# Performance work log

Hardware: AMD Instinct MI355X
Metric: run time of the kernel (lower is better)

## Reference

```python
import jax, jax.numpy as jnp
import numpy as np

B, S, H, DH = 1, 4096, 8, 40  # hardcoded in the original forward
D = H * DH  # 320

def setup_inputs() -> dict:
    key = jax.random.key(0)
    ks = jax.random.split(key, 6)
    s = 1.0 / np.sqrt(D)
    return {
        "x": jax.random.normal(ks[0], (B, S, D), dtype=jnp.float32),
        "Wq": jax.random.normal(ks[1], (D, D), dtype=jnp.float32) * s,
        "Wk": jax.random.normal(ks[2], (D, D), dtype=jnp.float32) * s,
        "Wv": jax.random.normal(ks[3], (D, D), dtype=jnp.float32) * s,
        "Wo": jax.random.normal(ks[4], (D, D), dtype=jnp.float32) * s,
        "bo": jnp.zeros((D,), dtype=jnp.float32),
    }

def reference(x, Wq, Wk, Wv, Wo, bo):
    scale = DH ** (-0.5)
    # nn.Linear(bias=False): y = x @ W^T. context = x (self-attention).
    q = x @ Wq.T
    k = x @ Wk.T
    v = x @ Wv.T
    # split heads: [B,S,D] -> [B*H, S, DH]
    def split_heads(t):
        return t.reshape(B, S, H, DH).transpose(0, 2, 1, 3).reshape(B * H, S, DH)
    q, k, v = split_heads(q), split_heads(k), split_heads(v)
    # fp32 QK^T (original forces float), softmax, AV
    sim = jnp.einsum('bid,bjd->bij', q.astype(jnp.float32), k.astype(jnp.float32)) * scale
    attn = jax.nn.softmax(sim, axis=-1)
    out = jnp.einsum('bij,bjd->bid', attn, v)
    # merge heads: [B*H, S, DH] -> [B, S, D]
    out = out.reshape(B, H, S, DH).transpose(0, 2, 1, 3).reshape(B, S, D)
    return out @ Wo.T + bo
```

## Files before the change

kernel.cpp:

```cpp
#include <hip/hip_runtime.h>
#include <math.h>


#define NS 4096
#define ND 320
#define SCALE2 0.2281101152f
#define HS48 196608
#define VTH 163840
#define XN 1310720
#define WN 102400

typedef __attribute__((ext_vector_type(8))) short bf16x8;
typedef __attribute__((ext_vector_type(16))) float f32x16;

static __device__ __forceinline__ unsigned short f2b(float f) {
  unsigned int u = __builtin_bit_cast(unsigned int, f);
  u += 0x7fffu + ((u >> 16) & 1u);
  return (unsigned short)(u >> 16);
}
static __device__ __forceinline__ unsigned int pk2rne(float a, float b) {
  return (unsigned int)f2b(a) | ((unsigned int)f2b(b) << 16);
}
static __device__ __forceinline__ unsigned int pk2t(float a, float b) {
  return __builtin_amdgcn_perm(__builtin_bit_cast(unsigned int, b),
                               __builtin_bit_cast(unsigned int, a), 0x07060302u);
}
static __device__ __forceinline__ bf16x8 ld8(const unsigned short* p) {
  union { uint2 u[2]; bf16x8 v; } c;
  c.u[0] = *(const uint2*)p;
  c.u[1] = *(const uint2*)(p + 4);
  return c.v;
}
static __device__ __forceinline__ void st16(unsigned short* p, uint4 v) {
  *(uint2*)p = make_uint2(v.x, v.y);
  *(uint2*)(p + 4) = make_uint2(v.z, v.w);
}

__global__ __launch_bounds__(256) void cvt_kernel(
    const float* __restrict__ x, const float* __restrict__ Wq,
    const float* __restrict__ Wk, const float* __restrict__ Wv,
    const float* __restrict__ Wo, unsigned short* __restrict__ dst) {
  int e = (blockIdx.x * 256 + threadIdx.x) * 4;
  const float* src; int off;
  if (e < XN)               { src = x;  off = e; }
  else if (e < XN + WN)     { src = Wq; off = e - XN; }
  else if (e < XN + 2 * WN) { src = Wk; off = e - XN - WN; }
  else if (e < XN + 3 * WN) { src = Wv; off = e - XN - 2 * WN; }
  else                      { src = Wo; off = e - XN - 3 * WN; }
  float4 v = *(const float4*)(src + off);
  *(uint2*)(dst + e) = make_uint2(pk2rne(v.x, v.y), pk2rne(v.z, v.w));
}

__global__ __launch_bounds__(256) void proj_qkv_kernel(
    const unsigned short* __restrict__ xb, const unsigned short* __restrict__ Wb,
    unsigned short* __restrict__ Qp, unsigned short* __restrict__ Kp,
    unsigned short* __restrict__ Vt) {
  const int z = blockIdx.z;
  const unsigned short* W = Wb + z * WN;
  __shared__ __align__(16) unsigned short As[64 * 36];
  __shared__ __align__(16) unsigned short Bs[64 * 36];
  const int t = threadIdx.x;
  const int w = t >> 6, l = t & 63, l31 = l & 31, hi = l >> 5;
  const int bm = blockIdx.x * 64, bn = blockIdx.y * 64;
  const int m0 = (w & 1) * 32, n0 = (w >> 1) * 32;
  f32x16 acc = {0,0,0,0,0,0,0,0,0,0,0,0,0,0,0,0};
  const int ar = t >> 2, ac = t & 3;
  const unsigned short* gA = xb + (bm + ar) * ND + ac * 8;
  const unsigned short* gB = W + (bn + ar) * ND + ac * 8;
  unsigned short* lA = As + ar * 36 + ac * 8;
  unsigned short* lB = Bs + ar * 36 + ac * 8;
  const unsigned short* af = As + (m0 + l31) * 36 + hi * 8;
  const unsigned short* bf = Bs + (n0 + l31) * 36 + hi * 8;
  for (int k0 = 0; k0 < ND; k0 += 32) {
    __syncthreads();
    uint4 a = *(const uint4*)gA;
    uint4 b = *(const uint4*)gB;
    st16(lA, a); st16(lB, b);
    gA += 32; gB += 32;
    __syncthreads();
    bf16x8 A0 = ld8(af), A1 = ld8(af + 16);
    bf16x8 B0 = ld8(bf), B1 = ld8(bf + 16);
    acc = __builtin_amdgcn_mfma_f32_32x32x16_bf16(A0, B0, acc, 0, 0, 0);
    acc = __builtin_amdgcn_mfma_f32_32x32x16_bf16(A1, B1, acc, 0, 0, 0);
  }
  const int j = bn + n0 + l31;
  const int h = j / 40, dh = j - h * 40;
  if (z < 2) {
    unsigned short* Y = (z == 0) ? Qp : Kp;
    const float sc = (z == 0) ? SCALE2 : 1.0f;
    const unsigned short padv = (z == 0) ? (unsigned short)0xC200u
                                         : (unsigned short)0x3F80u;
#pragma unroll
    for (int r = 0; r < 16; r++) {
      int row = bm + m0 + (r & 3) + 8 * (r >> 2) + 4 * hi;
      Y[h * HS48 + row * 48 + dh] = f2b(acc[r] * sc);
      if (dh < 8)
        Y[h * HS48 + row * 48 + 40 + dh] = (dh == 0) ? padv : (unsigned short)0;
    }
  } else {
#pragma unroll
    for (int r = 0; r < 16; r++) {
      int row = bm + m0 + (r & 3) + 8 * (r >> 2) + 4 * hi;
      Vt[h * VTH + dh * NS + row] = f2b(acc[r]);
    }
  }
}

__global__ __launch_bounds__(256, 4) void attn_kernel(
    const unsigned short* __restrict__ Qp, const unsigned short* __restrict__ Kp,
    const unsigned short* __restrict__ Vt, float* __restrict__ Op,
    float* __restrict__ Lp) {
  const int b = blockIdx.x;
  const int h = b & 7, ks = (b >> 3) & 3, qt = b >> 5;
  const int t = threadIdx.x;
  const int w = t >> 6, l = t & 63, l31 = l & 31, hi = l >> 5;
  __shared__ __align__(16) unsigned short Ks[128 * 68];
  __shared__ __align__(16) unsigned short Vs[48 * 132];
  if (t < 66) ((unsigned int*)(Vs + 40 * 132))[t] = 0x3F803F80u;

  const int kbase = ks * 1024;
  const int qbase = qt * 128 + w * 32;
  const unsigned short* qp = Qp + h * HS48 + (qbase + l31) * 48 + hi * 8;
  bf16x8 qf0 = *(const bf16x8*)qp;
  bf16x8 qf1 = *(const bf16x8*)(qp + 16);
  bf16x8 qf2 = *(const bf16x8*)(qp + 32);

  f32x16 oa0 = {0,0,0,0,0,0,0,0,0,0,0,0,0,0,0,0};
  f32x16 oa1 = {0,0,0,0,0,0,0,0,0,0,0,0,0,0,0,0};

  const int krow = t >> 1, khalf = t & 1;
  const unsigned short* gK = Kp + h * HS48 + (kbase + krow) * 48 + khalf * 24;
  unsigned short* lK = Ks + krow * 68 + khalf * 24;
  const int vg = t & 15;
  const int vr0 = t >> 4, vr1 = (t + 256) >> 4, vr2 = (t + 512) >> 4;
  const unsigned short* gV = Vt + h * VTH + kbase;

  for (int it = 0; it < 8; ++it) {
    __syncthreads();
    uint4 ka = *(const uint4*)gK;
    uint4 kb = *(const uint4*)(gK + 8);
    uint4 kc = *(const uint4*)(gK + 16);
    st16(lK, ka); st16(lK + 8, kb); st16(lK + 16, kc);
    uint4 v0 = *(const uint4*)(gV + vr0 * NS + vg * 8);
    uint4 v1 = *(const uint4*)(gV + vr1 * NS + vg * 8);
    st16(Vs + vr0 * 132 + vg * 8, v0);
    st16(Vs + vr1 * 132 + vg * 8, v1);
    if (t < 128) {
      uint4 v2 = *(const uint4*)(gV + vr2 * NS + vg * 8);
      st16(Vs + vr2 * 132 + vg * 8, v2);
    }
    gK += 128 * 48; gV += 128;
    __syncthreads();

#pragma unroll
    for (int half = 0; half < 2; ++half) {
      const unsigned short* kfb = Ks + (half * 64 + l31) * 68 + hi * 8;
      f32x16 s0 = {0,0,0,0,0,0,0,0,0,0,0,0,0,0,0,0};
      f32x16 s1 = {0,0,0,0,0,0,0,0,0,0,0,0,0,0,0,0};
      {
        bf16x8 k0 = ld8(kfb), k1 = ld8(kfb + 16), k2 = ld8(kfb + 32);
        s0 = __builtin_amdgcn_mfma_f32_32x32x16_bf16(k0, qf0, s0, 0, 0, 0);
        s0 = __builtin_amdgcn_mfma_f32_32x32x16_bf16(k1, qf1, s0, 0, 0, 0);
        s0 = __builtin_amdgcn_mfma_f32_32x32x16_bf16(k2, qf2, s0, 0, 0, 0);
      }
      {
        const unsigned short* kg = kfb + 32 * 68;
        bf16x8 k0 = ld8(kg), k1 = ld8(kg + 16), k2 = ld8(kg + 32);
        s1 = __builtin_amdgcn_mfma_f32_32x32x16_bf16(k0, qf0, s1, 0, 0, 0);
        s1 = __builtin_amdgcn_mfma_f32_32x32x16_bf16(k1, qf1, s1, 0, 0, 0);
        s1 = __builtin_amdgcn_mfma_f32_32x32x16_bf16(k2, qf2, s1, 0, 0, 0);
      }
      float p0[16], p1[16];
#pragma unroll
      for (int r = 0; r < 16; r++) {
        p0[r] = exp2f(s0[r]);
        p1[r] = exp2f(s1[r]);
      }
      unsigned int pw0[8], pw1[8];
#pragma unroll
      for (int g = 0; g < 4; g++) {
        pw0[2 * g]     = pk2t(p0[4 * g + 0], p0[4 * g + 1]);
        pw0[2 * g + 1] = pk2t(p0[4 * g + 2], p0[4 * g + 3]);
        pw1[2 * g]     = pk2t(p1[4 * g + 0], p1[4 * g + 1]);
        pw1[2 * g + 1] = pk2t(p1[4 * g + 2], p1[4 * g + 3]);
      }
      unsigned int s00 = hi ? pw0[0] : pw0[2], s01 = hi ? pw0[1] : pw0[3];
      unsigned int s02 = hi ? pw0[4] : pw0[6], s03 = hi ? pw0[5] : pw0[7];
      unsigned int s10 = hi ? pw1[0] : pw1[2], s11 = hi ? pw1[1] : pw1[3];
      unsigned int s12 = hi ? pw1[4] : pw1[6], s13 = hi ? pw1[5] : pw1[7];
      unsigned int r00 = __shfl_xor(s00, 32), r01 = __shfl_xor(s01, 32);
      unsigned int r02 = __shfl_xor(s02, 32), r03 = __shfl_xor(s03, 32);
      unsigned int r10 = __shfl_xor(s10, 32), r11 = __shfl_xor(s11, 32);
      unsigned int r12 = __shfl_xor(s12, 32), r13 = __shfl_xor(s13, 32);
      uint4 u0 = hi ? make_uint4(r00, r01, pw0[2], pw0[3])
                    : make_uint4(pw0[0], pw0[1], r00, r01);
      uint4 u1 = hi ? make_uint4(r02, r03, pw0[6], pw0[7])
                    : make_uint4(pw0[4], pw0[5], r02, r03);
      uint4 u2 = hi ? make_uint4(r10, r11, pw1[2], pw1[3])
                    : make_uint4(pw1[0], pw1[1], r10, r11);
      uint4 u3 = hi ? make_uint4(r12, r13, pw1[6], pw1[7])
                    : make_uint4(pw1[4], pw1[5], r12, r13);
      bf16x8 pf[4];
      pf[0] = __builtin_bit_cast(bf16x8, u0);
      pf[1] = __builtin_bit_cast(bf16x8, u1);
      pf[2] = __builtin_bit_cast(bf16x8, u2);
      pf[3] = __builtin_bit_cast(bf16x8, u3);

      const unsigned short* vfb = Vs + l31 * 132 + half * 64 + hi * 8;
      const unsigned short* vfb2 = Vs + (32 + (l31 & 15)) * 132 + half * 64 + hi * 8;
      const bf16x8 zf = {0, 0, 0, 0, 0, 0, 0, 0};
#pragma unroll
      for (int sub = 0; sub < 4; sub++) {
        bf16x8 vb0 = ld8(vfb + sub * 16);
        bf16x8 vb1t = ld8(vfb2 + sub * 16);
        bf16x8 vb1 = (l31 < 9) ? vb1t : zf;
        oa0 = __builtin_amdgcn_mfma_f32_32x32x16_bf16(pf[sub], vb0, oa0, 0, 0, 0);
        oa1 = __builtin_amdgcn_mfma_f32_32x32x16_bf16(pf[sub], vb1, oa1, 0, 0, 0);
      }
    }
  }
  float* opb = Op + ks * 1310720 + h * 163840;
  float* lpb = Lp + ks * 32768 + h * NS;
#pragma unroll
  for (int r = 0; r < 16; r++) {
    int qr = qbase + (r & 3) + 8 * (r >> 2) + 4 * hi;
    opb[qr * 40 + l31] = oa0[r];
    if (l31 < 8) opb[qr * 40 + 32 + l31] = oa1[r];
    if (l31 == 8) lpb[qr] = oa1[r];
  }
}

__global__ __launch_bounds__(256) void combine_kernel(
    const float* __restrict__ Op, const float* __restrict__ Lp,
    unsigned short* __restrict__ Xo) {
  int e = (blockIdx.x * 256 + threadIdx.x) * 2;
  int h = e / 163840;
  int r = e - h * 163840;
  int s = r / 40;
  int dh = r - s * 40;
  float2 a0 = *(const float2*)(Op + e);
  float2 a1 = *(const float2*)(Op + e + 1310720);
  float2 a2 = *(const float2*)(Op + e + 2621440);
  float2 a3 = *(const float2*)(Op + e + 3932160);
  int li = h * NS + s;
  float lsum = Lp[li] + Lp[li + 32768] + Lp[li + 65536] + Lp[li + 98304];
  float inv = 1.0f / lsum;
  float o0 = (a0.x + a1.x + a2.x + a3.x) * inv;
  float o1 = (a0.y + a1.y + a2.y + a3.y) * inv;
  *(unsigned int*)(Xo + s * ND + h * 40 + dh) = pk2rne(o0, o1);
}

__global__ __launch_bounds__(256) void proj_out_kernel(
    const unsigned short* __restrict__ Xo, const unsigned short* __restrict__ Wob,
    const float* __restrict__ bo, float* __restrict__ out) {
  __shared__ __align__(16) unsigned short As[64 * 36];
  __shared__ __align__(16) unsigned short Bs[64 * 36];
  const int t = threadIdx.x;
  const int w = t >> 6, l = t & 63, l31 = l & 31, hi = l >> 5;
  const int bm = blockIdx.x * 64, bn = blockIdx.y * 64;
  const int m0 = (w & 1) * 32, n0 = (w >> 1) * 32;
  f32x16 acc = {0,0,0,0,0,0,0,0,0,0,0,0,0,0,0,0};
  const int ar = t >> 2, ac = t & 3;
  const unsigned short* gA = Xo + (bm + ar) * ND + ac * 8;
  const unsigned short* gB = Wob + (bn + ar) * ND + ac * 8;
  unsigned short* lA = As + ar * 36 + ac * 8;
  unsigned short* lB = Bs + ar * 36 + ac * 8;
  const unsigned short* af = As + (m0 + l31) * 36 + hi * 8;
  const unsigned short* bf = Bs + (n0 + l31) * 36 + hi * 8;
  for (int k0 = 0; k0 < ND; k0 += 32) {
    __syncthreads();
    uint4 a = *(const uint4*)gA;
    uint4 b = *(const uint4*)gB;
    st16(lA, a); st16(lB, b);
    gA += 32; gB += 32;
    __syncthreads();
    bf16x8 A0 = ld8(af), A1 = ld8(af + 16);
    bf16x8 B0 = ld8(bf), B1 = ld8(bf + 16);
    acc = __builtin_amdgcn_mfma_f32_32x32x16_bf16(A0, B0, acc, 0, 0, 0);
    acc = __builtin_amdgcn_mfma_f32_32x32x16_bf16(A1, B1, acc, 0, 0, 0);
  }
  const int j = bn + n0 + l31;
  const float bj = bo[j];
#pragma unroll
  for (int r = 0; r < 16; r++) {
    int row = bm + m0 + (r & 3) + 8 * (r >> 2) + 4 * hi;
    out[row * ND + j] = acc[r] + bj;
  }
}

extern "C" void kernel_launch(void* const* d_in, const int* in_sizes, int n_in,
                              void* d_out, int out_size, void* d_ws, size_t ws_size,
                              hipStream_t stream) {
  (void)in_sizes; (void)n_in; (void)out_size; (void)ws_size;
  const float* x  = (const float*)d_in[0];
  const float* Wq = (const float*)d_in[1];
  const float* Wk = (const float*)d_in[2];
  const float* Wv = (const float*)d_in[3];
  const float* Wo = (const float*)d_in[4];
  const float* bo = (const float*)d_in[5];
  float* out = (float*)d_out;

  unsigned short* xb = (unsigned short*)d_ws;
  unsigned short* Wb = xb + XN;
  unsigned short* Qp = Wb + 4 * WN;
  unsigned short* Kp = Qp + 8 * HS48;
  unsigned short* Vt = Kp + 8 * HS48;
  unsigned short* Xo = Vt + 8 * VTH;
  float* Op = (float*)(Xo + XN);
  float* Lp = Op + 4 * 1310720;

  cvt_kernel<<<dim3(1680), 256, 0, stream>>>(x, Wq, Wk, Wv, Wo, xb);
  proj_qkv_kernel<<<dim3(64, 5, 3), 256, 0, stream>>>(xb, Wb, Qp, Kp, Vt);
  attn_kernel<<<dim3(1024), 256, 0, stream>>>(Qp, Kp, Vt, Op, Lp);
  combine_kernel<<<dim3(2560), 256, 0, stream>>>(Op, Lp, Xo);
  proj_out_kernel<<<dim3(64, 5), 256, 0, stream>>>(Xo, Wb + 3 * WN, bo, out);
}
```

Baseline: 140.0 us.

## Fuse fp32-to-bf16 conversion into GEMMs, split keys 8-way with bf16 partials

The separate conversion kernel is removed, and the QKV and output projections now load fp32 inputs and round them to bf16 while staging them into shared memory. The attention kernel now splits keys into 8 chunks using 64-key tiles, which doubles the grid. K rows are permuted as they are stored so the P fragments feed the PV MFMA directly, with no cross-lane shuffles. Partial outputs are stored in bf16 to cut write and read traffic, and the combine kernel sums 8 partials. The costs are more partial traffic per output element, extra rounding of the partial sums, and repeated fp32 loads of x and the weights across GEMM blocks.

New measurement: 145.8 us. 4.1% more time.

```diff
diff --git a/kernel.cpp b/kernel.cpp
--- a/kernel.cpp
+++ b/kernel.cpp
@@ -8,7 +8,6 @@
 #define HS48 196608
 #define VTH 163840
 #define XN 1310720
-#define WN 102400
 
 typedef __attribute__((ext_vector_type(8))) short bf16x8;
 typedef __attribute__((ext_vector_type(16))) float f32x16;
@@ -35,28 +34,18 @@
   *(uint2*)p = make_uint2(v.x, v.y);
   *(uint2*)(p + 4) = make_uint2(v.z, v.w);
 }
-
-__global__ __launch_bounds__(256) void cvt_kernel(
+static __device__ __forceinline__ int sig32(int q) {
+  int s = q >> 4, h2 = (q >> 3) & 1, j = q & 7;
+  return (s << 4) | ((j >> 2) << 3) | (h2 << 2) | (j & 3);
+}
+
+__global__ __launch_bounds__(256) void proj_qkv_kernel(
     const float* __restrict__ x, const float* __restrict__ Wq,
     const float* __restrict__ Wk, const float* __restrict__ Wv,
-    const float* __restrict__ Wo, unsigned short* __restrict__ dst) {
-  int e = (blockIdx.x * 256 + threadIdx.x) * 4;
-  const float* src; int off;
-  if (e < XN)               { src = x;  off = e; }
-  else if (e < XN + WN)     { src = Wq; off = e - XN; }
-  else if (e < XN + 2 * WN) { src = Wk; off = e - XN - WN; }
-  else if (e < XN + 3 * WN) { src = Wv; off = e - XN - 2 * WN; }
-  else                      { src = Wo; off = e - XN - 3 * WN; }
-  float4 v = *(const float4*)(src + off);
-  *(uint2*)(dst + e) = make_uint2(pk2rne(v.x, v.y), pk2rne(v.z, v.w));
-}
-
-__global__ __launch_bounds__(256) void proj_qkv_kernel(
-    const unsigned short* __restrict__ xb, const unsigned short* __restrict__ Wb,
     unsigned short* __restrict__ Qp, unsigned short* __restrict__ Kp,
     unsigned short* __restrict__ Vt) {
   const int z = blockIdx.z;
-  const unsigned short* W = Wb + z * WN;
+  const float* W = (z == 0) ? Wq : (z == 1) ? Wk : Wv;
   __shared__ __align__(16) unsigned short As[64 * 36];
   __shared__ __align__(16) unsigned short Bs[64 * 36];
   const int t = threadIdx.x;
@@ -65,17 +54,20 @@
   const int m0 = (w & 1) * 32, n0 = (w >> 1) * 32;
   f32x16 acc = {0,0,0,0,0,0,0,0,0,0,0,0,0,0,0,0};
   const int ar = t >> 2, ac = t & 3;
-  const unsigned short* gA = xb + (bm + ar) * ND + ac * 8;
-  const unsigned short* gB = W + (bn + ar) * ND + ac * 8;
+  const float* gA = x + (bm + ar) * ND + ac * 8;
+  const float* gB = W + (bn + ar) * ND + ac * 8;
   unsigned short* lA = As + ar * 36 + ac * 8;
   unsigned short* lB = Bs + ar * 36 + ac * 8;
   const unsigned short* af = As + (m0 + l31) * 36 + hi * 8;
   const unsigned short* bf = Bs + (n0 + l31) * 36 + hi * 8;
   for (int k0 = 0; k0 < ND; k0 += 32) {
     __syncthreads();
-    uint4 a = *(const uint4*)gA;
-    uint4 b = *(const uint4*)gB;
-    st16(lA, a); st16(lB, b);
+    float4 a0 = *(const float4*)gA, a1 = *(const float4*)(gA + 4);
+    float4 b0 = *(const float4*)gB, b1 = *(const float4*)(gB + 4);
+    st16(lA, make_uint4(pk2rne(a0.x, a0.y), pk2rne(a0.z, a0.w),
+                        pk2rne(a1.x, a1.y), pk2rne(a1.z, a1.w)));
+    st16(lB, make_uint4(pk2rne(b0.x, b0.y), pk2rne(b0.z, b0.w),
+                        pk2rne(b1.x, b1.y), pk2rne(b1.z, b1.w)));
     gA += 32; gB += 32;
     __syncthreads();
     bf16x8 A0 = ld8(af), A1 = ld8(af + 16);
@@ -106,19 +98,20 @@
   }
 }
 
-__global__ __launch_bounds__(256, 4) void attn_kernel(
+__global__ __launch_bounds__(256) void attn_kernel(
     const unsigned short* __restrict__ Qp, const unsigned short* __restrict__ Kp,
-    const unsigned short* __restrict__ Vt, float* __restrict__ Op,
+    const unsigned short* __restrict__ Vt, unsigned short* __restrict__ Op,
     float* __restrict__ Lp) {
   const int b = blockIdx.x;
-  const int h = b & 7, ks = (b >> 3) & 3, qt = b >> 5;
+  const int h = b & 7, ks = (b >> 3) & 7, qt = b >> 6;
   const int t = threadIdx.x;
   const int w = t >> 6, l = t & 63, l31 = l & 31, hi = l >> 5;
-  __shared__ __align__(16) unsigned short Ks[128 * 68];
-  __shared__ __align__(16) unsigned short Vs[48 * 132];
-  if (t < 66) ((unsigned int*)(Vs + 40 * 132))[t] = 0x3F803F80u;
-
-  const int kbase = ks * 1024;
+  __shared__ __align__(16) unsigned short Ks[64 * 68];
+  __shared__ __align__(16) unsigned short Vs[48 * 68];
+  for (int i = t; i < 272; i += 256)
+    ((unsigned int*)(Vs + 40 * 68))[i] = (i < 34) ? 0x3F803F80u : 0u;
+
+  const int kbase = ks * 512;
   const int qbase = qt * 128 + w * 32;
   const unsigned short* qp = Qp + h * HS48 + (qbase + l31) * 48 + hi * 8;
   bf16x8 qf0 = *(const bf16x8*)qp;
@@ -128,130 +121,100 @@
   f32x16 oa0 = {0,0,0,0,0,0,0,0,0,0,0,0,0,0,0,0};
   f32x16 oa1 = {0,0,0,0,0,0,0,0,0,0,0,0,0,0,0,0};
 
-  const int krow = t >> 1, khalf = t & 1;
-  const unsigned short* gK = Kp + h * HS48 + (kbase + krow) * 48 + khalf * 24;
-  unsigned short* lK = Ks + krow * 68 + khalf * 24;
-  const int vg = t & 15;
-  const int vr0 = t >> 4, vr1 = (t + 256) >> 4, vr2 = (t + 512) >> 4;
-  const unsigned short* gV = Vt + h * VTH + kbase;
+  const int kr0 = t / 6, kc0 = t - kr0 * 6;
+  const int kr1 = (t + 256) / 6, kc1 = (t + 256) - kr1 * 6;
+  const unsigned short* gK0 = Kp + h * HS48 + (kbase + kr0) * 48 + kc0 * 8;
+  const unsigned short* gK1 = Kp + h * HS48 + (kbase + kr1) * 48 + kc1 * 8;
+  unsigned short* lK0 = Ks + ((kr0 & 32) | sig32(kr0 & 31)) * 68 + kc0 * 8;
+  unsigned short* lK1 = Ks + ((kr1 & 32) | sig32(kr1 & 31)) * 68 + kc1 * 8;
+  const int vr0 = t >> 3, vc = t & 7, vr1 = 32 + vr0;
+  const unsigned short* gV0 = Vt + h * VTH + vr0 * NS + kbase + vc * 8;
+  const unsigned short* gV1 = Vt + h * VTH + vr1 * NS + kbase + vc * 8;
+  unsigned short* lV0 = Vs + vr0 * 68 + vc * 8;
+  unsigned short* lV1 = Vs + vr1 * 68 + vc * 8;
+
+  const unsigned short* kf0 = Ks + l31 * 68 + hi * 8;
+  const unsigned short* kf1 = Ks + (32 + l31) * 68 + hi * 8;
+  const unsigned short* vf0 = Vs + l31 * 68 + hi * 8;
+  const unsigned short* vf1 = Vs + (32 + (l31 & 15)) * 68 + hi * 8;
 
   for (int it = 0; it < 8; ++it) {
     __syncthreads();
-    uint4 ka = *(const uint4*)gK;
-    uint4 kb = *(const uint4*)(gK + 8);
-    uint4 kc = *(const uint4*)(gK + 16);
-    st16(lK, ka); st16(lK + 8, kb); st16(lK + 16, kc);
-    uint4 v0 = *(const uint4*)(gV + vr0 * NS + vg * 8);
-    uint4 v1 = *(const uint4*)(gV + vr1 * NS + vg * 8);
-    st16(Vs + vr0 * 132 + vg * 8, v0);
-    st16(Vs + vr1 * 132 + vg * 8, v1);
-    if (t < 128) {
-      uint4 v2 = *(const uint4*)(gV + vr2 * NS + vg * 8);
-      st16(Vs + vr2 * 132 + vg * 8, v2);
-    }
-    gK += 128 * 48; gV += 128;
-    __syncthreads();
-
-#pragma unroll
-    for (int half = 0; half < 2; ++half) {
-      const unsigned short* kfb = Ks + (half * 64 + l31) * 68 + hi * 8;
+    uint4 ka = *(const uint4*)gK0;
+    st16(lK0, ka);
+    if (t < 128) { uint4 kb2 = *(const uint4*)gK1; st16(lK1, kb2); }
+    uint4 va = *(const uint4*)gV0;
+    st16(lV0, va);
+    if (t < 64) { uint4 vb2 = *(const uint4*)gV1; st16(lV1, vb2); }
+    gK0 += 64 * 48; gK1 += 64 * 48; gV0 += 64; gV1 += 64;
+    __syncthreads();
+
+    unsigned int pw0[8], pw1[8];
+    {
       f32x16 s0 = {0,0,0,0,0,0,0,0,0,0,0,0,0,0,0,0};
+      s0 = __builtin_amdgcn_mfma_f32_32x32x16_bf16(ld8(kf0), qf0, s0, 0, 0, 0);
+      s0 = __builtin_amdgcn_mfma_f32_32x32x16_bf16(ld8(kf0 + 16), qf1, s0, 0, 0, 0);
+      s0 = __builtin_amdgcn_mfma_f32_32x32x16_bf16(ld8(kf0 + 32), qf2, s0, 0, 0, 0);
+#pragma unroll
+      for (int i = 0; i < 8; i++)
+        pw0[i] = pk2t(exp2f(s0[2 * i]), exp2f(s0[2 * i + 1]));
+    }
+    {
       f32x16 s1 = {0,0,0,0,0,0,0,0,0,0,0,0,0,0,0,0};
-      {
-        bf16x8 k0 = ld8(kfb), k1 = ld8(kfb + 16), k2 = ld8(kfb + 32);
-        s0 = __builtin_amdgcn_mfma_f32_32x32x16_bf16(k0, qf0, s0, 0, 0, 0);
-        s0 = __builtin_amdgcn_mfma_f32_32x32x16_bf16(k1, qf1, s0, 0, 0, 0);
-        s0 = __builtin_amdgcn_mfma_f32_32x32x16_bf16(k2, qf2, s0, 0, 0, 0);
-      }
-      {
-        const unsigned short* kg = kfb + 32 * 68;
-        bf16x8 k0 = ld8(kg), k1 = ld8(kg + 16), k2 = ld8(kg + 32);
-        s1 = __builtin_amdgcn_mfma_f32_32x32x16_bf16(k0, qf0, s1, 0, 0, 0);
-        s1 = __builtin_amdgcn_mfma_f32_32x32x16_bf16(k1, qf1, s1, 0, 0, 0);
-        s1 = __builtin_amdgcn_mfma_f32_32x32x16_bf16(k2, qf2, s1, 0, 0, 0);
-      }
-      float p0[16], p1[16];
-#pragma unroll
-      for (int r = 0; r < 16; r++) {
-        p0[r] = exp2f(s0[r]);
-        p1[r] = exp2f(s1[r]);
-      }
-      unsigned int pw0[8], pw1[8];
-#pragma unroll
-      for (int g = 0; g < 4; g++) {
-        pw0[2 * g]     = pk2t(p0[4 * g + 0], p0[4 * g + 1]);
-        pw0[2 * g + 1] = pk2t(p0[4 * g + 2], p0[4 * g + 3]);
-        pw1[2 * g]     = pk2t(p1[4 * g + 0], p1[4 * g + 1]);
-        pw1[2 * g + 1] = pk2t(p1[4 * g + 2], p1[4 * g + 3]);
-      }
-      unsigned int s00 = hi ? pw0[0] : pw0[2], s01 = hi ? pw0[1] : pw0[3];
-      unsigned int s02 = hi ? pw0[4] : pw0[6], s03 = hi ? pw0[5] : pw0[7];
-      unsigned int s10 = hi ? pw1[0] : pw1[2], s11 = hi ? pw1[1] : pw1[3];
-      unsigned int s12 = hi ? pw1[4] : pw1[6], s13 = hi ? pw1[5] : pw1[7];
-      unsigned int r00 = __shfl_xor(s00, 32), r01 = __shfl_xor(s01, 32);
-      unsigned int r02 = __shfl_xor(s02, 32), r03 = __shfl_xor(s03, 32);
-      unsigned int r10 = __shfl_xor(s10, 32), r11 = __shfl_xor(s11, 32);
-      unsigned int r12 = __shfl_xor(s12, 32), r13 = __shfl_xor(s13, 32);
-      uint4 u0 = hi ? make_uint4(r00, r01, pw0[2], pw0[3])
-                    : make_uint4(pw0[0], pw0[1], r00, r01);
-      uint4 u1 = hi ? make_uint4(r02, r03, pw0[6], pw0[7])
-                    : make_uint4(pw0[4], pw0[5], r02, r03);
-      uint4 u2 = hi ? make_uint4(r10, r11, pw1[2], pw1[3])
-                    : make_uint4(pw1[0], pw1[1], r10, r11);
-      uint4 u3 = hi ? make_uint4(r12, r13, pw1[6], pw1[7])
-                    : make_uint4(pw1[4], pw1[5], r12, r13);
-      bf16x8 pf[4];
-      pf[0] = __builtin_bit_cast(bf16x8, u0);
-      pf[1] = __builtin_bit_cast(bf16x8, u1);
-      pf[2] = __builtin_bit_cast(bf16x8, u2);
-      pf[3] = __builtin_bit_cast(bf16x8, u3);
-
-      const unsigned short* vfb = Vs + l31 * 132 + half * 64 + hi * 8;
-      const unsigned short* vfb2 = Vs + (32 + (l31 & 15)) * 132 + half * 64 + hi * 8;
-      const bf16x8 zf = {0, 0, 0, 0, 0, 0, 0, 0};
-#pragma unroll
-      for (int sub = 0; sub < 4; sub++) {
-        bf16x8 vb0 = ld8(vfb + sub * 16);
-        bf16x8 vb1t = ld8(vfb2 + sub * 16);
-        bf16x8 vb1 = (l31 < 9) ? vb1t : zf;
-        oa0 = __builtin_amdgcn_mfma_f32_32x32x16_bf16(pf[sub], vb0, oa0, 0, 0, 0);
-        oa1 = __builtin_amdgcn_mfma_f32_32x32x16_bf16(pf[sub], vb1, oa1, 0, 0, 0);
-      }
-    }
-  }
-  float* opb = Op + ks * 1310720 + h * 163840;
+      s1 = __builtin_amdgcn_mfma_f32_32x32x16_bf16(ld8(kf1), qf0, s1, 0, 0, 0);
+      s1 = __builtin_amdgcn_mfma_f32_32x32x16_bf16(ld8(kf1 + 16), qf1, s1, 0, 0, 0);
+      s1 = __builtin_amdgcn_mfma_f32_32x32x16_bf16(ld8(kf1 + 32), qf2, s1, 0, 0, 0);
+#pragma unroll
+      for (int i = 0; i < 8; i++)
+        pw1[i] = pk2t(exp2f(s1[2 * i]), exp2f(s1[2 * i + 1]));
+    }
+    bf16x8 pf0 = __builtin_bit_cast(bf16x8, make_uint4(pw0[0], pw0[1], pw0[2], pw0[3]));
+    bf16x8 pf1 = __builtin_bit_cast(bf16x8, make_uint4(pw0[4], pw0[5], pw0[6], pw0[7]));
+    bf16x8 pf2 = __builtin_bit_cast(bf16x8, make_uint4(pw1[0], pw1[1], pw1[2], pw1[3]));
+    bf16x8 pf3 = __builtin_bit_cast(bf16x8, make_uint4(pw1[4], pw1[5], pw1[6], pw1[7]));
+    oa0 = __builtin_amdgcn_mfma_f32_32x32x16_bf16(pf0, ld8(vf0), oa0, 0, 0, 0);
+    oa1 = __builtin_amdgcn_mfma_f32_32x32x16_bf16(pf0, ld8(vf1), oa1, 0, 0, 0);
+    oa0 = __builtin_amdgcn_mfma_f32_32x32x16_bf16(pf1, ld8(vf0 + 16), oa0, 0, 0, 0);
+    oa1 = __builtin_amdgcn_mfma_f32_32x32x16_bf16(pf1, ld8(vf1 + 16), oa1, 0, 0, 0);
+    oa0 = __builtin_amdgcn_mfma_f32_32x32x16_bf16(pf2, ld8(vf0 + 32), oa0, 0, 0, 0);
+    oa1 = __builtin_amdgcn_mfma_f32_32x32x16_bf16(pf2, ld8(vf1 + 32), oa1, 0, 0, 0);
+    oa0 = __builtin_amdgcn_mfma_f32_32x32x16_bf16(pf3, ld8(vf0 + 48), oa0, 0, 0, 0);
+    oa1 = __builtin_amdgcn_mfma_f32_32x32x16_bf16(pf3, ld8(vf1 + 48), oa1, 0, 0, 0);
+  }
+
+  unsigned short* opb = Op + ks * 1310720 + h * 163840;
   float* lpb = Lp + ks * 32768 + h * NS;
 #pragma unroll
   for (int r = 0; r < 16; r++) {
     int qr = qbase + (r & 3) + 8 * (r >> 2) + 4 * hi;
-    opb[qr * 40 + l31] = oa0[r];
-    if (l31 < 8) opb[qr * 40 + 32 + l31] = oa1[r];
+    opb[qr * 40 + l31] = f2b(oa0[r]);
+    if (l31 < 8) opb[qr * 40 + 32 + l31] = f2b(oa1[r]);
     if (l31 == 8) lpb[qr] = oa1[r];
   }
 }
 
 __global__ __launch_bounds__(256) void combine_kernel(
-    const float* __restrict__ Op, const float* __restrict__ Lp,
+    const unsigned short* __restrict__ Op, const float* __restrict__ Lp,
     unsigned short* __restrict__ Xo) {
   int e = (blockIdx.x * 256 + threadIdx.x) * 2;
   int h = e / 163840;
   int r = e - h * 163840;
   int s = r / 40;
   int dh = r - s * 40;
-  float2 a0 = *(const float2*)(Op + e);
-  float2 a1 = *(const float2*)(Op + e + 1310720);
-  float2 a2 = *(const float2*)(Op + e + 2621440);
-  float2 a3 = *(const float2*)(Op + e + 3932160);
-  int li = h * NS + s;
-  float lsum = Lp[li] + Lp[li + 32768] + Lp[li + 65536] + Lp[li + 98304];
+  float a0 = 0.f, a1 = 0.f, lsum = 0.f;
+#pragma unroll
+  for (int k = 0; k < 8; k++) {
+    unsigned int u = *(const unsigned int*)(Op + k * 1310720 + e);
+    a0 += __builtin_bit_cast(float, u << 16);
+    a1 += __builtin_bit_cast(float, u & 0xFFFF0000u);
+    lsum += Lp[k * 32768 + h * NS + s];
+  }
   float inv = 1.0f / lsum;
-  float o0 = (a0.x + a1.x + a2.x + a3.x) * inv;
-  float o1 = (a0.y + a1.y + a2.y + a3.y) * inv;
-  *(unsigned int*)(Xo + s * ND + h * 40 + dh) = pk2rne(o0, o1);
+  *(unsigned int*)(Xo + s * ND + h * 40 + dh) = pk2rne(a0 * inv, a1 * inv);
 }
 
 __global__ __launch_bounds__(256) void proj_out_kernel(
-    const unsigned short* __restrict__ Xo, const unsigned short* __restrict__ Wob,
+    const unsigned short* __restrict__ Xo, const float* __restrict__ Wo,
     const float* __restrict__ bo, float* __restrict__ out) {
   __shared__ __align__(16) unsigned short As[64 * 36];
   __shared__ __align__(16) unsigned short Bs[64 * 36];
@@ -262,7 +225,7 @@
   f32x16 acc = {0,0,0,0,0,0,0,0,0,0,0,0,0,0,0,0};
   const int ar = t >> 2, ac = t & 3;
   const unsigned short* gA = Xo + (bm + ar) * ND + ac * 8;
-  const unsigned short* gB = Wob + (bn + ar) * ND + ac * 8;
+  const float* gB = Wo + (bn + ar) * ND + ac * 8;
   unsigned short* lA = As + ar * 36 + ac * 8;
   unsigned short* lB = Bs + ar * 36 + ac * 8;
   const unsigned short* af = As + (m0 + l31) * 36 + hi * 8;
@@ -270,8 +233,10 @@
   for (int k0 = 0; k0 < ND; k0 += 32) {
     __syncthreads();
     uint4 a = *(const uint4*)gA;
-    uint4 b = *(const uint4*)gB;
-    st16(lA, a); st16(lB, b);
+    float4 b0 = *(const float4*)gB, b1 = *(const float4*)(gB + 4);
+    st16(lA, a);
+    st16(lB, make_uint4(pk2rne(b0.x, b0.y), pk2rne(b0.z, b0.w),
+                        pk2rne(b1.x, b1.y), pk2rne(b1.z, b1.w)));
     gA += 32; gB += 32;
     __syncthreads();
     bf16x8 A0 = ld8(af), A1 = ld8(af + 16);
@@ -300,18 +265,15 @@
   const float* bo = (const float*)d_in[5];
   float* out = (float*)d_out;
 
-  unsigned short* xb = (unsigned short*)d_ws;
-  unsigned short* Wb = xb + XN;
-  unsigned short* Qp = Wb + 4 * WN;
+  unsigned short* Qp = (unsigned short*)d_ws;
   unsigned short* Kp = Qp + 8 * HS48;
   unsigned short* Vt = Kp + 8 * HS48;
   unsigned short* Xo = Vt + 8 * VTH;
-  float* Op = (float*)(Xo + XN);
-  float* Lp = Op + 4 * 1310720;
-
-  cvt_kernel<<<dim3(1680), 256, 0, stream>>>(x, Wq, Wk, Wv, Wo, xb);
-  proj_qkv_kernel<<<dim3(64, 5, 3), 256, 0, stream>>>(xb, Wb, Qp, Kp, Vt);
-  attn_kernel<<<dim3(1024), 256, 0, stream>>>(Qp, Kp, Vt, Op, Lp);
+  unsigned short* Op = Xo + XN;
+  float* Lp = (float*)(Op + 8 * XN);
+
+  proj_qkv_kernel<<<dim3(64, 5, 3), 256, 0, stream>>>(x, Wq, Wk, Wv, Qp, Kp, Vt);
+  attn_kernel<<<dim3(2048), 256, 0, stream>>>(Qp, Kp, Vt, Op, Lp);
   combine_kernel<<<dim3(2560), 256, 0, stream>>>(Op, Lp, Xo);
-  proj_out_kernel<<<dim3(64, 5), 256, 0, stream>>>(Xo, Wb + 3 * WN, bo, out);
-}
+  proj_out_kernel<<<dim3(64, 5), 256, 0, stream>>>(Xo, Wo, bo, out);
+}
```
